# Optimization experiments

Hardware: AMD Instinct MI355X
Metric: run time of the kernel (lower is better)

## Reference

```python
import jax, jax.numpy as jnp
import numpy as np

NUM_ITEMS = 100000
EMB_DIM = 128
HALF = EMB_DIM // 2
MAX_ITEMS = 200
BATCH = 16384


def setup_inputs() -> dict:
    key = jax.random.key(0)
    ks = jax.random.split(key, 16)
    inp = {
        "ratings": jax.random.uniform(ks[0], (BATCH, MAX_ITEMS), jnp.float32) * 5.0,
        "item_ids": jax.random.randint(ks[1], (BATCH, MAX_ITEMS), 0, NUM_ITEMS),
        "noise": jax.random.normal(ks[2], (BATCH, EMB_DIM), jnp.float32),
        "init_user_emb": jax.random.normal(ks[3], (BATCH, EMB_DIM), jnp.float32),
        # embedding tables (embedding_dim=4)
        "gmf_emb": jax.random.normal(ks[4], (NUM_ITEMS, 4), jnp.float32) * 0.1,
        "ncf_emb": jax.random.normal(ks[5], (NUM_ITEMS, 4), jnp.float32) * 0.1,
        # four Linear(HALF, 4) layers (kaiming-normal-ish weights, zero bias)
        "W0": jax.random.normal(ks[6], (4, HALF), jnp.float32) * np.sqrt(2.0 / 4),
        "b0": jnp.zeros((4,), jnp.float32),
        "W1": jax.random.normal(ks[7], (4, HALF), jnp.float32) * np.sqrt(2.0 / 4),
        "b1": jnp.zeros((4,), jnp.float32),
        "W2": jax.random.normal(ks[8], (4, HALF), jnp.float32) * np.sqrt(2.0 / 4),
        "b2": jnp.zeros((4,), jnp.float32),
        "W3": jax.random.normal(ks[9], (4, HALF), jnp.float32) * np.sqrt(2.0 / 4),
        "b3": jnp.zeros((4,), jnp.float32),
        # ncf_layers: Linear(12, 8) + ReLU
        "Wn": jax.random.normal(ks[10], (8, 12), jnp.float32) * 0.2,
        "bn": jnp.zeros((8,), jnp.float32),
        # final_layer: Linear(16, 1)
        "Wf": jax.random.normal(ks[11], (1, 16), jnp.float32) * 0.2,
        "bf": jnp.zeros((1,), jnp.float32),
        # learned mixing scalar p
        "p": jnp.ones((1,), jnp.float32),
    }
    return inp


def _forward(ratings, item_ids, noise, init_user_emb,
             gmf_emb, ncf_emb, W0, b0, W1, b1, W2, b2, W3, b3,
             Wn, bn, Wf, bf, p):
    # embedding lookups: [B, M, 4]
    gmf_item = gmf_emb[item_ids]
    ncf_item = ncf_emb[item_ids]
    # split user emb / noise into gmf, ncf halves: [B, HALF] each
    gmf_user, ncf_user = init_user_emb[:, :HALF], init_user_emb[:, HALF:]
    gmf_noise, ncf_noise = noise[:, :HALF], noise[:, HALF:]
    # tiny projections to dim 4
    gmf_user = gmf_user @ W0.T + b0        # [B, 4]
    ncf_user = ncf_user @ W1.T + b1        # [B, 4]
    gmf_noise = gmf_noise @ W2.T + b2      # [B, 4]
    ncf_noise = ncf_noise @ W3.T + b3      # [B, 4]
    # einsum 'ijk,ik->ijk': elementwise scale by broadcast
    gmf_noise_e = gmf_item * gmf_noise[:, None, :]   # [B, M, 4]
    gmf_user_e = gmf_item * gmf_user[:, None, :]     # [B, M, 4]
    gmf_out = jnp.concatenate([gmf_user_e, gmf_noise_e], axis=-1)  # [B, M, 8]
    # broadcast ncf user/noise over items, concat with item embs: [B, M, 12]
    B, M = item_ids.shape
    ncf_in = jnp.concatenate([
        jnp.broadcast_to(ncf_user[:, None, :], (B, M, 4)),
        jnp.broadcast_to(ncf_noise[:, None, :], (B, M, 4)),
        ncf_item,
    ], axis=-1)
    ncf_out = jax.nn.relu(ncf_in @ Wn.T + bn)        # [B, M, 8]
    comb = jnp.concatenate([gmf_out, ncf_out], axis=-1)  # [B, M, 16]
    score = (comb @ Wf.T + bf)[..., 0]               # [B, M]
    return p * ratings + score


def reference(ratings, item_ids, noise, init_user_emb,
              gmf_emb, ncf_emb, W0, b0, W1, b1, W2, b2, W3, b3,
              Wn, bn, Wf, bf, p):
    return _forward(ratings, item_ids, noise, init_user_emb,
                    gmf_emb, ncf_emb, W0, b0, W1, b1, W2, b2, W3, b3,
                    Wn, bn, Wf, bf, p)
```

## Files before the change

kernel.cpp:

```cpp
#include <hip/hip_runtime.h>
#include <hip/hip_bf16.h>

#define BATCH 16384
#define MAX_ITEMS 200
#define TOTAL (BATCH * MAX_ITEMS)

__global__ __launch_bounds__(256) void user_precompute(
    const float* __restrict__ noise,
    const float* __restrict__ uemb,
    const float* __restrict__ W0, const float* __restrict__ b0,
    const float* __restrict__ W1, const float* __restrict__ b1,
    const float* __restrict__ W2, const float* __restrict__ b2,
    const float* __restrict__ W3, const float* __restrict__ b3,
    const float* __restrict__ Wn, const float* __restrict__ bn,
    const float* __restrict__ Wf,
    float* __restrict__ ws)
{
    int wid  = (blockIdx.x * blockDim.x + threadIdx.x) >> 6;
    int lane = threadIdx.x & 63;
    if (wid >= BATCH) return;

    const float* ur = uemb  + (size_t)wid * 128;
    const float* nr = noise + (size_t)wid * 128;
    float e0 = ur[lane];
    float e1 = ur[64 + lane];
    float n0 = nr[lane];
    float n1 = nr[64 + lane];

    float gu[4], nu[4], gn[4], nn[4];
#pragma unroll
    for (int j = 0; j < 4; ++j) {
        float a = e0 * W0[j * 64 + lane];
        float b = e1 * W1[j * 64 + lane];
        float c = n0 * W2[j * 64 + lane];
        float d = n1 * W3[j * 64 + lane];
#pragma unroll
        for (int m = 1; m < 64; m <<= 1) {
            a += __shfl_xor(a, m, 64);
            b += __shfl_xor(b, m, 64);
            c += __shfl_xor(c, m, 64);
            d += __shfl_xor(d, m, 64);
        }
        gu[j] = a + b0[j];
        nu[j] = b + b1[j];
        gn[j] = c + b2[j];
        nn[j] = d + b3[j];
    }

    if (lane == 0) {
        float* o = ws + (size_t)wid * 12;
#pragma unroll
        for (int j = 0; j < 4; ++j)
            o[j] = Wf[j] * gu[j] + Wf[4 + j] * gn[j];
#pragma unroll
        for (int k = 0; k < 8; ++k) {
            float t = bn[k];
#pragma unroll
            for (int i = 0; i < 4; ++i)
                t += Wn[k * 12 + i] * nu[i] + Wn[k * 12 + 4 + i] * nn[i];
            o[4 + k] = t;
        }
    }
}

__global__ __launch_bounds__(256) void score_kernel(
    const float* __restrict__ ratings,
    const int*   __restrict__ ids,
    const float* __restrict__ gmf_emb,
    const float* __restrict__ ncf_emb,
    const float* __restrict__ Wn,
    const float* __restrict__ Wf,
    const float* __restrict__ bf,
    const float* __restrict__ p,
    const float* __restrict__ ws,
    float* __restrict__ out)
{
    __shared__ float sWn[32];
    __shared__ float sWf[8];
    __shared__ float sBF, sP;

    int tid = threadIdx.x;
    if (tid < 32)      sWn[tid] = Wn[(tid >> 2) * 12 + 8 + (tid & 3)];
    else if (tid < 40) sWf[tid - 32] = Wf[8 + (tid - 32)];
    else if (tid == 40) sBF = bf[0];
    else if (tid == 41) sP  = p[0];
    __syncthreads();

    int idx = blockIdx.x * blockDim.x + tid;
    if (idx >= TOTAL) return;

    int b = idx / MAX_ITEMS;

    float rating = ratings[idx];
    int   id     = ids[idx];

    const float4 gi = *reinterpret_cast<const float4*>(gmf_emb + (size_t)id * 4);
    const float4 ni = *reinterpret_cast<const float4*>(ncf_emb + (size_t)id * 4);

    const float* u = ws + (size_t)b * 12;
    float acc = sBF
              + gi.x * u[0] + gi.y * u[1] + gi.z * u[2] + gi.w * u[3];

#pragma unroll
    for (int k = 0; k < 8; ++k) {
        float t = u[4 + k]
                + sWn[k * 4 + 0] * ni.x
                + sWn[k * 4 + 1] * ni.y
                + sWn[k * 4 + 2] * ni.z
                + sWn[k * 4 + 3] * ni.w;
        acc += sWf[k] * fmaxf(t, 0.0f);
    }

    out[idx] = sP * rating + acc;
}

extern "C" void kernel_launch(void* const* d_in, const int* in_sizes, int n_in,
                              void* d_out, int out_size, void* d_ws, size_t ws_size,
                              hipStream_t stream) {
    const float* ratings = (const float*)d_in[0];
    const int*   ids     = (const int*)  d_in[1];
    const float* noise   = (const float*)d_in[2];
    const float* uemb    = (const float*)d_in[3];
    const float* gmf_emb = (const float*)d_in[4];
    const float* ncf_emb = (const float*)d_in[5];
    const float* W0 = (const float*)d_in[6];
    const float* b0 = (const float*)d_in[7];
    const float* W1 = (const float*)d_in[8];
    const float* b1 = (const float*)d_in[9];
    const float* W2 = (const float*)d_in[10];
    const float* b2 = (const float*)d_in[11];
    const float* W3 = (const float*)d_in[12];
    const float* b3 = (const float*)d_in[13];
    const float* Wn = (const float*)d_in[14];
    const float* bn = (const float*)d_in[15];
    const float* Wf = (const float*)d_in[16];
    const float* bf = (const float*)d_in[17];
    const float* p  = (const float*)d_in[18];
    float* out = (float*)d_out;
    float* ws  = (float*)d_ws;

    user_precompute<<<BATCH / 4, 256, 0, stream>>>(
        noise, uemb, W0, b0, W1, b1, W2, b2, W3, b3, Wn, bn, Wf, ws);

    score_kernel<<<(TOTAL + 255) / 256, 256, 0, stream>>>(
        ratings, ids, gmf_emb, ncf_emb, Wn, Wf, bf, p, ws, out);
}
```

Before: 163.6 us.

## Fuse user projection and item scoring into one kernel with one block per user

Merges the per-user projection kernel and the per-item scoring kernel into a single launch where each 256-thread block handles one user. The four waves each compute one of the four projections, share them through shared memory, and then score the user's 200 items. This removes the second launch and the workspace round-trip through global memory. In exchange, 56 of 256 threads sit idle during scoring, the block needs a barrier, and every thread redundantly recomputes the 12 per-user coefficients.

```diff
diff --git a/kernel.cpp b/kernel.cpp
--- a/kernel.cpp
+++ b/kernel.cpp
@@ -3,115 +3,100 @@
 
 #define BATCH 16384
 #define MAX_ITEMS 200
-#define TOTAL (BATCH * MAX_ITEMS)
 
-__global__ __launch_bounds__(256) void user_precompute(
+__global__ __launch_bounds__(256) void ncf_fused(
+    const float* __restrict__ ratings,
+    const int*   __restrict__ ids,
     const float* __restrict__ noise,
     const float* __restrict__ uemb,
+    const float* __restrict__ gmf_emb,
+    const float* __restrict__ ncf_emb,
     const float* __restrict__ W0, const float* __restrict__ b0,
     const float* __restrict__ W1, const float* __restrict__ b1,
     const float* __restrict__ W2, const float* __restrict__ b2,
     const float* __restrict__ W3, const float* __restrict__ b3,
     const float* __restrict__ Wn, const float* __restrict__ bn,
-    const float* __restrict__ Wf,
-    float* __restrict__ ws)
+    const float* __restrict__ Wf, const float* __restrict__ bf,
+    const float* __restrict__ p,
+    float* __restrict__ out)
 {
-    int wid  = (blockIdx.x * blockDim.x + threadIdx.x) >> 6;
-    int lane = threadIdx.x & 63;
-    if (wid >= BATCH) return;
+    __shared__ float sproj[16];
 
-    const float* ur = uemb  + (size_t)wid * 128;
-    const float* nr = noise + (size_t)wid * 128;
-    float e0 = ur[lane];
-    float e1 = ur[64 + lane];
-    float n0 = nr[lane];
-    float n1 = nr[64 + lane];
+    const int u    = blockIdx.x;
+    const int tid  = threadIdx.x;
+    const int wave = tid >> 6;
+    const int lane = tid & 63;
 
-    float gu[4], nu[4], gn[4], nn[4];
+    const bool active = tid < MAX_ITEMS;
+    const size_t idx  = (size_t)u * MAX_ITEMS + tid;
+    float rating = 0.0f;
+    int   id     = 0;
+    if (active) {
+        rating = ratings[idx];
+        id     = ids[idx];
+    }
+
+    const float* Wsel;
+    const float* bsel;
+    const float* src;
+    if      (wave == 0) { Wsel = W0; bsel = b0; src = uemb  + (size_t)u * 128;      }
+    else if (wave == 1) { Wsel = W1; bsel = b1; src = uemb  + (size_t)u * 128 + 64; }
+    else if (wave == 2) { Wsel = W2; bsel = b2; src = noise + (size_t)u * 128;      }
+    else                { Wsel = W3; bsel = b3; src = noise + (size_t)u * 128 + 64; }
+
+    float x = src[lane];
 #pragma unroll
     for (int j = 0; j < 4; ++j) {
-        float a = e0 * W0[j * 64 + lane];
-        float b = e1 * W1[j * 64 + lane];
-        float c = n0 * W2[j * 64 + lane];
-        float d = n1 * W3[j * 64 + lane];
+        float s = x * Wsel[j * 64 + lane];
 #pragma unroll
-        for (int m = 1; m < 64; m <<= 1) {
-            a += __shfl_xor(a, m, 64);
-            b += __shfl_xor(b, m, 64);
-            c += __shfl_xor(c, m, 64);
-            d += __shfl_xor(d, m, 64);
-        }
-        gu[j] = a + b0[j];
-        nu[j] = b + b1[j];
-        gn[j] = c + b2[j];
-        nn[j] = d + b3[j];
+        for (int m = 1; m < 64; m <<= 1)
+            s += __shfl_xor(s, m, 64);
+        if (lane == 0)
+            sproj[wave * 4 + j] = s + bsel[j];
     }
 
-    if (lane == 0) {
-        float* o = ws + (size_t)wid * 12;
+    float4 gi = make_float4(0.f, 0.f, 0.f, 0.f);
+    float4 ni = make_float4(0.f, 0.f, 0.f, 0.f);
+    if (active) {
+        gi = *reinterpret_cast<const float4*>(gmf_emb + (size_t)id * 4);
+        ni = *reinterpret_cast<const float4*>(ncf_emb + (size_t)id * 4);
+    }
+
+    __syncthreads();
+
+    float pr[16];
 #pragma unroll
-        for (int j = 0; j < 4; ++j)
-            o[j] = Wf[j] * gu[j] + Wf[4 + j] * gn[j];
+    for (int i = 0; i < 16; ++i) pr[i] = sproj[i];
+
+    float uu[4];
+#pragma unroll
+    for (int j = 0; j < 4; ++j)
+        uu[j] = Wf[j] * pr[j] + Wf[4 + j] * pr[8 + j];
+
+    float base[8];
+#pragma unroll
+    for (int k = 0; k < 8; ++k) {
+        float t = bn[k];
+#pragma unroll
+        for (int i = 0; i < 4; ++i)
+            t += Wn[k * 12 + i] * pr[4 + i] + Wn[k * 12 + 4 + i] * pr[12 + i];
+        base[k] = t;
+    }
+
+    if (active) {
+        float acc = bf[0]
+                  + gi.x * uu[0] + gi.y * uu[1] + gi.z * uu[2] + gi.w * uu[3];
 #pragma unroll
         for (int k = 0; k < 8; ++k) {
-            float t = bn[k];
-#pragma unroll
-            for (int i = 0; i < 4; ++i)
-                t += Wn[k * 12 + i] * nu[i] + Wn[k * 12 + 4 + i] * nn[i];
-            o[4 + k] = t;
+            float t = base[k]
+                    + Wn[k * 12 + 8]  * ni.x
+                    + Wn[k * 12 + 9]  * ni.y
+                    + Wn[k * 12 + 10] * ni.z
+                    + Wn[k * 12 + 11] * ni.w;
+            acc += Wf[8 + k] * fmaxf(t, 0.0f);
         }
+        out[idx] = p[0] * rating + acc;
     }
-}
-
-__global__ __launch_bounds__(256) void score_kernel(
-    const float* __restrict__ ratings,
-    const int*   __restrict__ ids,
-    const float* __restrict__ gmf_emb,
-    const float* __restrict__ ncf_emb,
-    const float* __restrict__ Wn,
-    const float* __restrict__ Wf,
-    const float* __restrict__ bf,
-    const float* __restrict__ p,
-    const float* __restrict__ ws,
-    float* __restrict__ out)
-{
-    __shared__ float sWn[32];
-    __shared__ float sWf[8];
-    __shared__ float sBF, sP;
-
-    int tid = threadIdx.x;
-    if (tid < 32)      sWn[tid] = Wn[(tid >> 2) * 12 + 8 + (tid & 3)];
-    else if (tid < 40) sWf[tid - 32] = Wf[8 + (tid - 32)];
-    else if (tid == 40) sBF = bf[0];
-    else if (tid == 41) sP  = p[0];
-    __syncthreads();
-
-    int idx = blockIdx.x * blockDim.x + tid;
-    if (idx >= TOTAL) return;
-
-    int b = idx / MAX_ITEMS;
-
-    float rating = ratings[idx];
-    int   id     = ids[idx];
-
-    const float4 gi = *reinterpret_cast<const float4*>(gmf_emb + (size_t)id * 4);
-    const float4 ni = *reinterpret_cast<const float4*>(ncf_emb + (size_t)id * 4);
-
-    const float* u = ws + (size_t)b * 12;
-    float acc = sBF
-              + gi.x * u[0] + gi.y * u[1] + gi.z * u[2] + gi.w * u[3];
-
-#pragma unroll
-    for (int k = 0; k < 8; ++k) {
-        float t = u[4 + k]
-                + sWn[k * 4 + 0] * ni.x
-                + sWn[k * 4 + 1] * ni.y
-                + sWn[k * 4 + 2] * ni.z
-                + sWn[k * 4 + 3] * ni.w;
-        acc += sWf[k] * fmaxf(t, 0.0f);
-    }
-
-    out[idx] = sP * rating + acc;
 }
 
 extern "C" void kernel_launch(void* const* d_in, const int* in_sizes, int n_in,
@@ -137,11 +122,8 @@
     const float* bf = (const float*)d_in[17];
     const float* p  = (const float*)d_in[18];
     float* out = (float*)d_out;
-    float* ws  = (float*)d_ws;
 
-    user_precompute<<<BATCH / 4, 256, 0, stream>>>(
-        noise, uemb, W0, b0, W1, b1, W2, b2, W3, b3, Wn, bn, Wf, ws);
-
-    score_kernel<<<(TOTAL + 255) / 256, 256, 0, stream>>>(
-        ratings, ids, gmf_emb, ncf_emb, Wn, Wf, bf, p, ws, out);
+    ncf_fused<<<BATCH, 256, 0, stream>>>(
+        ratings, ids, noise, uemb, gmf_emb, ncf_emb,
+        W0, b0, W1, b1, W2, b2, W3, b3, Wn, bn, Wf, bf, p, out);
 }
```

After: 168.2 us. 1.03x slower.

## Vectorize score kernel to four items per thread and tile user projection

Applied to the files above, without the earlier changes.

The score kernel now processes four consecutive items per thread, using float4/int4 loads for ratings and ids and a float4 store for outputs. Each thread also fetches the per-user precomputed coefficients once as float4s, which relies on MAX_ITEMS being divisible by 4. The user precompute kernel changes from one wave per user with shuffle reductions to 64 users per block, with the projection weights staged in shared memory and four threads per user computing dot products serially. The aim is fewer memory instructions and less index math per item, and removal of the shuffle-reduction overhead, at the cost of higher register use per thread.

```diff
diff --git a/kernel.cpp b/kernel.cpp
--- a/kernel.cpp
+++ b/kernel.cpp
@@ -4,6 +4,8 @@
 #define BATCH 16384
 #define MAX_ITEMS 200
 #define TOTAL (BATCH * MAX_ITEMS)
+#define A_USERS 64
+#define B_ITEMS 4
 
 __global__ __launch_bounds__(256) void user_precompute(
     const float* __restrict__ noise,
@@ -16,54 +18,75 @@
     const float* __restrict__ Wf,
     float* __restrict__ ws)
 {
-    int wid  = (blockIdx.x * blockDim.x + threadIdx.x) >> 6;
-    int lane = threadIdx.x & 63;
-    if (wid >= BATCH) return;
+    __shared__ float sW[16 * 68];
+    __shared__ float sproj[A_USERS * 17];
 
-    const float* ur = uemb  + (size_t)wid * 128;
-    const float* nr = noise + (size_t)wid * 128;
-    float e0 = ur[lane];
-    float e1 = ur[64 + lane];
-    float n0 = nr[lane];
-    float n1 = nr[64 + lane];
+    const int tid = threadIdx.x;
 
-    float gu[4], nu[4], gn[4], nn[4];
+    for (int k = tid; k < 1024; k += 256) {
+        int row = k >> 6;
+        int i   = k & 63;
+        int r   = row >> 2;
+        int j   = row & 3;
+        const float* Wr = (r == 0) ? W0 : (r == 1) ? W1 : (r == 2) ? W2 : W3;
+        sW[row * 68 + i] = Wr[j * 64 + i];
+    }
+    __syncthreads();
+
+    const int u_local = tid >> 2;
+    const int r       = tid & 3;
+    const int u       = blockIdx.x * A_USERS + u_local;
+
+    const float* srcbase = (r < 2) ? uemb : noise;
+    const float4* src = reinterpret_cast<const float4*>(
+        srcbase + (size_t)u * 128 + (r & 1) * 64);
+
+    const float4* w0p = reinterpret_cast<const float4*>(&sW[(r * 4 + 0) * 68]);
+    const float4* w1p = reinterpret_cast<const float4*>(&sW[(r * 4 + 1) * 68]);
+    const float4* w2p = reinterpret_cast<const float4*>(&sW[(r * 4 + 2) * 68]);
+    const float4* w3p = reinterpret_cast<const float4*>(&sW[(r * 4 + 3) * 68]);
+
+    float a0 = 0.f, a1 = 0.f, a2 = 0.f, a3 = 0.f;
 #pragma unroll
-    for (int j = 0; j < 4; ++j) {
-        float a = e0 * W0[j * 64 + lane];
-        float b = e1 * W1[j * 64 + lane];
-        float c = n0 * W2[j * 64 + lane];
-        float d = n1 * W3[j * 64 + lane];
+    for (int i4 = 0; i4 < 16; ++i4) {
+        float4 x  = src[i4];
+        float4 w0 = w0p[i4];
+        float4 w1 = w1p[i4];
+        float4 w2 = w2p[i4];
+        float4 w3 = w3p[i4];
+        a0 += x.x * w0.x + x.y * w0.y + x.z * w0.z + x.w * w0.w;
+        a1 += x.x * w1.x + x.y * w1.y + x.z * w1.z + x.w * w1.w;
+        a2 += x.x * w2.x + x.y * w2.y + x.z * w2.z + x.w * w2.w;
+        a3 += x.x * w3.x + x.y * w3.y + x.z * w3.z + x.w * w3.w;
+    }
+    const float* br = (r == 0) ? b0 : (r == 1) ? b1 : (r == 2) ? b2 : b3;
+    sproj[u_local * 17 + r * 4 + 0] = a0 + br[0];
+    sproj[u_local * 17 + r * 4 + 1] = a1 + br[1];
+    sproj[u_local * 17 + r * 4 + 2] = a2 + br[2];
+    sproj[u_local * 17 + r * 4 + 3] = a3 + br[3];
+    __syncthreads();
+
+    if (tid < A_USERS) {
+        float pr[16];
 #pragma unroll
-        for (int m = 1; m < 64; m <<= 1) {
-            a += __shfl_xor(a, m, 64);
-            b += __shfl_xor(b, m, 64);
-            c += __shfl_xor(c, m, 64);
-            d += __shfl_xor(d, m, 64);
-        }
-        gu[j] = a + b0[j];
-        nu[j] = b + b1[j];
-        gn[j] = c + b2[j];
-        nn[j] = d + b3[j];
-    }
+        for (int c = 0; c < 16; ++c) pr[c] = sproj[tid * 17 + c];
 
-    if (lane == 0) {
-        float* o = ws + (size_t)wid * 12;
+        float* o = ws + (size_t)(blockIdx.x * A_USERS + tid) * 12;
 #pragma unroll
         for (int j = 0; j < 4; ++j)
-            o[j] = Wf[j] * gu[j] + Wf[4 + j] * gn[j];
+            o[j] = Wf[j] * pr[j] + Wf[4 + j] * pr[8 + j];
 #pragma unroll
         for (int k = 0; k < 8; ++k) {
             float t = bn[k];
 #pragma unroll
             for (int i = 0; i < 4; ++i)
-                t += Wn[k * 12 + i] * nu[i] + Wn[k * 12 + 4 + i] * nn[i];
+                t += Wn[k * 12 + i] * pr[4 + i] + Wn[k * 12 + 4 + i] * pr[12 + i];
             o[4 + k] = t;
         }
     }
 }
 
-__global__ __launch_bounds__(256) void score_kernel(
+__global__ __launch_bounds__(256) void score4(
     const float* __restrict__ ratings,
     const int*   __restrict__ ids,
     const float* __restrict__ gmf_emb,
@@ -79,39 +102,58 @@
     __shared__ float sWf[8];
     __shared__ float sBF, sP;
 
-    int tid = threadIdx.x;
-    if (tid < 32)      sWn[tid] = Wn[(tid >> 2) * 12 + 8 + (tid & 3)];
-    else if (tid < 40) sWf[tid - 32] = Wf[8 + (tid - 32)];
+    const int tid = threadIdx.x;
+    if (tid < 32)       sWn[tid] = Wn[(tid >> 2) * 12 + 8 + (tid & 3)];
+    else if (tid < 40)  sWf[tid - 32] = Wf[8 + (tid - 32)];
     else if (tid == 40) sBF = bf[0];
     else if (tid == 41) sP  = p[0];
     __syncthreads();
 
-    int idx = blockIdx.x * blockDim.x + tid;
-    if (idx >= TOTAL) return;
+    const int t = blockIdx.x * 256 + tid;
+    const int u = t / (MAX_ITEMS / B_ITEMS);
 
-    int b = idx / MAX_ITEMS;
+    float4 r4  = reinterpret_cast<const float4*>(ratings)[t];
+    int4   id4 = reinterpret_cast<const int4*>(ids)[t];
 
-    float rating = ratings[idx];
-    int   id     = ids[idx];
+    float4 gi0 = *reinterpret_cast<const float4*>(gmf_emb + (size_t)id4.x * 4);
+    float4 gi1 = *reinterpret_cast<const float4*>(gmf_emb + (size_t)id4.y * 4);
+    float4 gi2 = *reinterpret_cast<const float4*>(gmf_emb + (size_t)id4.z * 4);
+    float4 gi3 = *reinterpret_cast<const float4*>(gmf_emb + (size_t)id4.w * 4);
+    float4 ni0 = *reinterpret_cast<const float4*>(ncf_emb + (size_t)id4.x * 4);
+    float4 ni1 = *reinterpret_cast<const float4*>(ncf_emb + (size_t)id4.y * 4);
+    float4 ni2 = *reinterpret_cast<const float4*>(ncf_emb + (size_t)id4.z * 4);
+    float4 ni3 = *reinterpret_cast<const float4*>(ncf_emb + (size_t)id4.w * 4);
 
-    const float4 gi = *reinterpret_cast<const float4*>(gmf_emb + (size_t)id * 4);
-    const float4 ni = *reinterpret_cast<const float4*>(ncf_emb + (size_t)id * 4);
+    const float4* wsu = reinterpret_cast<const float4*>(ws + (size_t)u * 12);
+    float4 c0 = wsu[0];
+    float4 c1 = wsu[1];
+    float4 c2 = wsu[2];
+    const float base[8] = {c1.x, c1.y, c1.z, c1.w, c2.x, c2.y, c2.z, c2.w};
 
-    const float* u = ws + (size_t)b * 12;
-    float acc = sBF
-              + gi.x * u[0] + gi.y * u[1] + gi.z * u[2] + gi.w * u[3];
+    const float4 gis[4] = {gi0, gi1, gi2, gi3};
+    const float4 nis[4] = {ni0, ni1, ni2, ni3};
+    const float  rr[4]  = {r4.x, r4.y, r4.z, r4.w};
+    float res[4];
 
 #pragma unroll
-    for (int k = 0; k < 8; ++k) {
-        float t = u[4 + k]
-                + sWn[k * 4 + 0] * ni.x
-                + sWn[k * 4 + 1] * ni.y
-                + sWn[k * 4 + 2] * ni.z
-                + sWn[k * 4 + 3] * ni.w;
-        acc += sWf[k] * fmaxf(t, 0.0f);
+    for (int e = 0; e < 4; ++e) {
+        float4 gi = gis[e];
+        float4 ni = nis[e];
+        float acc = sBF
+                  + gi.x * c0.x + gi.y * c0.y + gi.z * c0.z + gi.w * c0.w;
+#pragma unroll
+        for (int k = 0; k < 8; ++k) {
+            float tv = base[k]
+                     + sWn[k * 4 + 0] * ni.x
+                     + sWn[k * 4 + 1] * ni.y
+                     + sWn[k * 4 + 2] * ni.z
+                     + sWn[k * 4 + 3] * ni.w;
+            acc += sWf[k] * fmaxf(tv, 0.0f);
+        }
+        res[e] = sP * rr[e] + acc;
     }
 
-    out[idx] = sP * rating + acc;
+    reinterpret_cast<float4*>(out)[t] = make_float4(res[0], res[1], res[2], res[3]);
 }
 
 extern "C" void kernel_launch(void* const* d_in, const int* in_sizes, int n_in,
@@ -139,9 +181,9 @@
     float* out = (float*)d_out;
     float* ws  = (float*)d_ws;
 
-    user_precompute<<<BATCH / 4, 256, 0, stream>>>(
+    user_precompute<<<BATCH / A_USERS, 256, 0, stream>>>(
         noise, uemb, W0, b0, W1, b1, W2, b2, W3, b3, Wn, bn, Wf, ws);
 
-    score_kernel<<<(TOTAL + 255) / 256, 256, 0, stream>>>(
+    score4<<<TOTAL / B_ITEMS / 256, 256, 0, stream>>>(
         ratings, ids, gmf_emb, ncf_emb, Wn, Wf, bf, p, ws, out);
 }
```

New measurement: 152.0 us. 1.08x faster.
